# Kernel optimization log

Hardware: AMD Instinct MI355X
Metric: run time of the kernel (lower is better)

## Reference

```python
import jax, jax.numpy as jnp
import numpy as np

AXES = 72        # NUM_OF_IMU_AXES
PARAMS = 12      # NUM_OF_NOISE_PARAMS
MAX_PROP = 600   # max_propogation
LN_EPS = 1e-5    # nn.LayerNorm default eps


def setup_inputs() -> dict:
    key = jax.random.key(0)
    k0, k1 = jax.random.split(key, 2)
    S, D = 4096, 512
    hidden_states = jax.random.normal(k0, (1, S, D), jnp.float32)
    gamma = jnp.ones((D,), jnp.float32)          # LayerNorm weight
    beta = jnp.zeros((D,), jnp.float32)          # LayerNorm bias
    W = jax.random.normal(k1, (D, AXES * PARAMS), jnp.float32) * 0.02  # Linear weight (in,out)
    b = jnp.zeros((AXES * PARAMS,), jnp.float32)
    return {"hidden_states": hidden_states, "gamma": gamma, "beta": beta, "W": W, "b": b}


def reference(hidden_states, gamma, beta, W, b):
    S = hidden_states.shape[1]
    T = min(MAX_PROP, S)  # time_steps_propogate_kinematics (static under jit)

    # LayerNorm over last dim
    x = hidden_states[0]  # (S, D); B == 1 by contract
    mu = jnp.mean(x, axis=-1, keepdims=True)
    var = jnp.mean((x - mu) ** 2, axis=-1, keepdims=True)
    xn = (x - mu) / jnp.sqrt(var + LN_EPS) * gamma + beta

    # Linear -> (seq, params, axes); rearrange 'seq (params axes)' => params outer
    p = (xn @ W + b).reshape(S, PARAMS, AXES)
    sp = jax.nn.softplus

    c, c_th = p[:, 4], p[:, 5]          # (S, A)
    phi, phi_th = p[:, 6], p[:, 7]
    d = sp(p[:, 1]); k = d * d / 4 + sp(p[:, 0])
    d_th = sp(p[:, 3]); k_th = d_th * d_th / 4 + sp(p[:, 2])

    acc_base = p[:, 8].T                # (A, S)
    acc_std = sp(p[:, 9]).T
    gyro_base = p[:, 10].T
    gyro_std = sp(p[:, 11]).T

    t = jnp.arange(T, dtype=jnp.float32)[None, :, None]  # (1, T, 1)

    def osc(cc, dd, kk, ph):
        # damped oscillator value grid, vectorized over all 72 axes: (S, T, A)
        om = jnp.sqrt(4.0 * kk - dd * dd) / 2.0  # = sqrt(softplus)>=0, safe
        return (cc[:, None, :] * jnp.exp(-dd[:, None, :] / 2.0 * t)
                * jnp.sin(t * om[:, None, :] + ph[:, None, :]))

    vals = osc(c, d, k, phi) + osc(c_th, d_th, k_th, phi_th)  # (S, T, A)

    # banded overlap-add: out[s + t] += vals[s, t]; positions >= S are dropped
    pos = (jnp.arange(S)[:, None] + jnp.arange(T)[None, :]).reshape(-1)  # (S*T,)
    vals_flat = vals.reshape(S * T, AXES)
    out = jnp.zeros((S + T, AXES), vals.dtype).at[pos].add(vals_flat)[:S]  # (S, A)
    kinematics = out.T  # (A, S)

    return kinematics, acc_base, acc_std, gyro_base, gyro_std
```

## Files before the change

### kernel.cpp

```cpp
#include <hip/hip_runtime.h>
#include <math.h>

#define S_TOTAL 4096
#define DDIM    512
#define AXES    72
#define NPROJ   864
#define T_PROP  600
#define SA      (S_TOTAL*AXES)
#define LN_EPS  1e-5f
#define AMP_CUT 4e-6f

typedef __attribute__((ext_vector_type(8))) short short8;
typedef __attribute__((ext_vector_type(4))) float f32x4;

__device__ __forceinline__ float softplus_f(float x) {
    return fmaxf(x, 0.f) + log1pf(expf(-fabsf(x)));
}
__device__ __forceinline__ unsigned short bf_hi(float f) {
    return (unsigned short)(__float_as_uint(f) >> 16);
}

__global__ __launch_bounds__(256) void prep_kernel(
        const float* __restrict__ x, const float* __restrict__ gamma,
        const float* __restrict__ beta, const float* __restrict__ W,
        unsigned short* __restrict__ Ahi, unsigned short* __restrict__ Alo,
        unsigned short* __restrict__ WhiT,
        float* __restrict__ kin) {
    __shared__ float Wt[32][33];
    int tid = threadIdx.x;
    int b = blockIdx.x;
    if (b < 1024) {
        int lane = tid & 63, w = tid >> 6;
        int row = b*4 + w;
        const float4* xr = reinterpret_cast<const float4*>(x + (size_t)row * DDIM);
        float4 xv[2] = { xr[lane], xr[lane + 64] };
        float sum = 0.f, ssq = 0.f;
#pragma unroll
        for (int c = 0; c < 2; ++c) {
            sum += (xv[c].x + xv[c].y) + (xv[c].z + xv[c].w);
            ssq += xv[c].x*xv[c].x + xv[c].y*xv[c].y + xv[c].z*xv[c].z + xv[c].w*xv[c].w;
        }
#pragma unroll
        for (int off = 1; off < 64; off <<= 1) {
            sum += __shfl_xor(sum, off);
            ssq += __shfl_xor(ssq, off);
        }
        float m = sum * (1.f/DDIM);
        float r = rsqrtf(ssq * (1.f/DDIM) - m*m + LN_EPS);
        const float4* gp = reinterpret_cast<const float4*>(gamma);
        const float4* bp = reinterpret_cast<const float4*>(beta);
#pragma unroll
        for (int c = 0; c < 2; ++c) {
            float4 gv = gp[lane + 64*c], bv = bp[lane + 64*c];
            float xn[4] = {(xv[c].x-m)*r*gv.x+bv.x, (xv[c].y-m)*r*gv.y+bv.y,
                           (xv[c].z-m)*r*gv.z+bv.z, (xv[c].w-m)*r*gv.w+bv.w};
            ushort4 h4, l4;
            unsigned short* hp = &h4.x;
            unsigned short* lp = &l4.x;
#pragma unroll
            for (int j = 0; j < 4; ++j) {
                unsigned short hi = bf_hi(xn[j]);
                float fhi = __uint_as_float((unsigned)hi << 16);
                hp[j] = hi;
                lp[j] = bf_hi(xn[j] - fhi);
            }
            size_t o = (size_t)row*DDIM + 256*c + lane*4;
            *reinterpret_cast<ushort4*>(&Ahi[o]) = h4;
            *reinterpret_cast<ushort4*>(&Alo[o]) = l4;
        }
    } else if (b < 1456) {
        int wb = b - 1024;
        int bk = wb / 27, bn = wb - bk*27;
        int tx = tid & 31, ty0 = tid >> 5;
#pragma unroll
        for (int rr = 0; rr < 4; ++rr) {
            int ty = ty0 + rr*8;
            Wt[ty][tx] = W[(size_t)(bk*32 + ty)*NPROJ + bn*32 + tx];
        }
        __syncthreads();
#pragma unroll
        for (int rr = 0; rr < 4; ++rr) {
            int ny = ty0 + rr*8;
            int n = bn*32 + ny;
            int k = bk*32 + tx;
            float f = Wt[tx][ny];
            WhiT[(size_t)n*DDIM + k] = bf_hi(f);
        }
    } else {
        int zb = b - 1456;
        float4 z4 = make_float4(0.f, 0.f, 0.f, 0.f);
        float4* kp = reinterpret_cast<float4*>(kin);
#pragma unroll
        for (int i = 0; i < 8; ++i)
            kp[zb*2048 + i*256 + tid] = z4;
    }
}

__global__ __launch_bounds__(256) void gemm_kernel(
        const unsigned short* __restrict__ Ahi, const unsigned short* __restrict__ Alo,
        const unsigned short* __restrict__ WhiT,
        const float* __restrict__ bias,
        float* __restrict__ P, float* __restrict__ out) {
    __shared__ __align__(16) unsigned short ldsArena[2*10240];

    int tid  = threadIdx.x;
    int lane = tid & 63;
    int wv   = tid >> 6;
    int wm   = wv & 1;
    int wn   = wv >> 1;
    int sBase = blockIdx.x * 32;
    int nBase = blockIdx.y * 96;
    int l15 = lane & 15;
    int g   = lane >> 4;
    int r7  = l15 & 7;

    int rr = lane >> 3;
    int jj = ((lane & 7) ^ rr) * 8;
    const unsigned short* gp[5];
#pragma unroll
    for (int sg = 0; sg < 5; ++sg) {
        int seg = wv*5 + sg;
        const unsigned short* src;
        int row;
        if (seg < 8) {
            int p = seg >> 2, rg = seg & 3;
            row = sBase + rg*8 + rr;
            src = p ? Alo : Ahi;
        } else {
            int rg = seg - 8;
            row = nBase + rg*8 + rr;
            src = WhiT;
        }
        gp[sg] = src + (size_t)row*DDIM + jj;
    }

    int koff0 = (g*16) ^ (r7<<4);
    int koff1 = (64 + g*16) ^ (r7<<4);
    int rowXb = (wm*16 + l15) * 128;
    int rowWb[3];
#pragma unroll
    for (int nf = 0; nf < 3; ++nf) rowWb[nf] = (wn*48 + nf*16 + l15) * 128;

    f32x4 acc[3] = {};

#define STAGE(buf, kt) do {                                                   \
        unsigned short* lb = ldsArena + (buf)*10240 + wv*2560;                \
        _Pragma("unroll")                                                     \
        for (int sg = 0; sg < 5; ++sg)                                        \
            __builtin_amdgcn_global_load_lds(                                 \
                (const __attribute__((address_space(1))) void*)(gp[sg] + (kt)*64), \
                (__attribute__((address_space(3))) void*)(lb + sg*512),       \
                16, 0, 0);                                                    \
    } while (0)

#define COMPUTE(BUF) do {                                                     \
        const char* Bc = (const char*)ldsArena + (BUF)*20480;                 \
        _Pragma("unroll")                                                     \
        for (int kk = 0; kk < 2; ++kk) {                                      \
            int ko = kk ? koff1 : koff0;                                      \
            short8 xh, xl, wh[3];                                             \
            xh = *reinterpret_cast<const short8*>(Bc + rowXb + ko);           \
            xl = *reinterpret_cast<const short8*>(Bc + 4096 + rowXb + ko);    \
            _Pragma("unroll")                                                 \
            for (int nf = 0; nf < 3; ++nf)                                    \
                wh[nf] = *reinterpret_cast<const short8*>(Bc + 8192 + rowWb[nf] + ko); \
            _Pragma("unroll")                                                 \
            for (int nf = 0; nf < 3; ++nf)                                    \
                acc[nf] = __builtin_amdgcn_mfma_f32_16x16x32_bf16(wh[nf], xh, acc[nf], 0, 0, 0); \
            _Pragma("unroll")                                                 \
            for (int nf = 0; nf < 3; ++nf)                                    \
                acc[nf] = __builtin_amdgcn_mfma_f32_16x16x32_bf16(wh[nf], xl, acc[nf], 0, 0, 0); \
        }                                                                     \
    } while (0)

    STAGE(0, 0);
    STAGE(1, 1);

#pragma unroll 1
    for (int kt2 = 0; kt2 < 4; ++kt2) {
        asm volatile("s_waitcnt vmcnt(5)" ::: "memory");
        __builtin_amdgcn_sched_barrier(0);
        __builtin_amdgcn_s_barrier();
        COMPUTE(0);
        __builtin_amdgcn_s_barrier();
        if (kt2 < 3) STAGE(0, 2*kt2 + 2);
        if (kt2 < 3) { asm volatile("s_waitcnt vmcnt(5)" ::: "memory"); }
        else         { asm volatile("s_waitcnt vmcnt(0)" ::: "memory"); }
        __builtin_amdgcn_sched_barrier(0);
        __builtin_amdgcn_s_barrier();
        COMPUTE(1);
        __builtin_amdgcn_s_barrier();
        if (kt2 < 3) STAGE(1, 2*kt2 + 3);
    }
#undef STAGE
#undef COMPUTE

    int s = sBase + wm*16 + l15;
    int nRowBase = nBase + wn*48 + (g<<2);
#pragma unroll
    for (int nf = 0; nf < 3; ++nf) {
#pragma unroll
        for (int r = 0; r < 4; ++r) {
            int n = nRowBase + nf*16 + r;
            float val = acc[nf][r] + bias[n];
            int ip = (n * 3641) >> 18;
            int a  = n - ip * 72;
            float res;
            if (ip == 0 || ip == 2)      res = sqrtf(softplus_f(val));
            else if (ip == 1 || ip == 3 || ip == 9 || ip == 11) res = softplus_f(val);
            else                          res = val;
            float* dst = (ip < 8) ? (P + (size_t)ip * SA)
                                  : (out + (size_t)(ip - 7) * SA);
            dst[(size_t)a * S_TOTAL + s] = res;
        }
    }
}

template<int STEPS>
__device__ __forceinline__ void osc_chunk(
        float& v1a, float& v1b, float& v2a, float& v2b,
        float p1, float q1, float p2, float q2,
        float& acc0, float& acc1, int lane, int lane4) {
#pragma unroll
    for (int i = 0; i < STEPS/2; ++i) {
        {
            const int dt = 2*i;
            v1b = fmaf(p1, v1a, -(q1*v1b));
            v2b = fmaf(p2, v2a, -(q2*v2b));
            float v = v1b + v2b;
            if (dt == 0) {
                acc0 += v;
            } else {
                int addr = (lane4 + (((64-dt)&63)<<2)) & 255;
                float vr = __int_as_float(__builtin_amdgcn_ds_bpermute(addr, __float_as_int(v)));
                bool nw = lane >= dt;
                acc0 += nw ? vr : 0.f;
                acc1 += nw ? 0.f : vr;
            }
        }
        {
            const int dt = 2*i + 1;
            v1a = fmaf(p1, v1b, -(q1*v1a));
            v2a = fmaf(p2, v2b, -(q2*v2a));
            float v = v1a + v2a;
            int addr = (lane4 + (((64-dt)&63)<<2)) & 255;
            float vr = __int_as_float(__builtin_amdgcn_ds_bpermute(addr, __float_as_int(v)));
            bool nw = lane >= dt;
            acc0 += nw ? vr : 0.f;
            acc1 += nw ? 0.f : vr;
        }
    }
}

__global__ __launch_bounds__(256) void osc_kernel(const float* __restrict__ P,
                                                  float* __restrict__ kin) {
    int tid  = threadIdx.x;
    int lane = tid & 63;
    int wv   = tid >> 6;
    int lane4 = lane << 2;
    int sBase = blockIdx.x * 64;
    int a  = blockIdx.y * 2 + (wv >> 1);
    int t0 = (wv & 1) * 300;
    float t0f = (float)t0;
    if (sBase + t0 >= S_TOTAL) return;

    size_t base = (size_t)a * S_TOTAL + sBase + lane;
    float om1 = P[0*(size_t)SA + base], d1 = P[1*(size_t)SA + base];
    float om2 = P[2*(size_t)SA + base], d2 = P[3*(size_t)SA + base];
    float c1  = P[4*(size_t)SA + base], c2  = P[5*(size_t)SA + base];
    float ph1 = P[6*(size_t)SA + base], ph2 = P[7*(size_t)SA + base];

    float dcf1 = __expf(-0.5f*d1);
    float e1   = c1 * __expf(-0.5f*d1*t0f);
    float s0, c0, so, co;
    __sincosf(fmaf(t0f, om1, ph1), &s0, &c0);
    __sincosf(om1, &so, &co);
    float inv1 = __expf(0.5f*d1);
    float p1 = 2.f*dcf1*co, q1 = dcf1*dcf1;
    float v1a = e1*inv1*(s0*co - c0*so);
    float cs2 = fmaf(2.f*co, co, -1.f), sn2 = 2.f*so*co;
    float v1b = e1*inv1*inv1*(s0*cs2 - c0*sn2);
    float amp1 = fabsf(e1);
    float dq1 = q1*q1; dq1*=dq1; dq1*=dq1; dq1*=dq1; dq1*=dq1;
    float dcf2 = __expf(-0.5f*d2);
    float e2   = c2 * __expf(-0.5f*d2*t0f);
    __sincosf(fmaf(t0f, om2, ph2), &s0, &c0);
    __sincosf(om2, &so, &co);
    float inv2 = __expf(0.5f*d2);
    float p2 = 2.f*dcf2*co, q2 = dcf2*dcf2;
    float v2a = e2*inv2*(s0*co - c0*so);
    cs2 = fmaf(2.f*co, co, -1.f); sn2 = 2.f*so*co;
    float v2b = e2*inv2*inv2*(s0*cs2 - c0*sn2);
    float amp2 = fabsf(e2);
    float dq2 = q2*q2; dq2*=dq2; dq2*=dq2; dq2*=dq2; dq2*=dq2;

    float acc0 = 0.f, acc1 = 0.f;
    float* kinA = kin + (size_t)a * S_TOTAL;
    int jBase = sBase + t0;
    int ran = 0;

#pragma unroll 1
    for (int c = 0; c < 5; ++c) {
        if (__all(fmaxf(amp1, amp2) < AMP_CUT)) break;
        if (c < 4) osc_chunk<64>(v1a, v1b, v2a, v2b, p1, q1, p2, q2, acc0, acc1, lane, lane4);
        else       osc_chunk<44>(v1a, v1b, v2a, v2b, p1, q1, p2, q2, acc0, acc1, lane, lane4);
        int j = jBase + lane;
        if (j < S_TOTAL) unsafeAtomicAdd(&kinA[j], acc0);
        acc0 = acc1; acc1 = 0.f;
        jBase += 64;
        amp1 *= dq1; amp2 *= dq2;
        ran = 1;
        if (jBase >= S_TOTAL) { ran = 0; break; }
    }
    if (ran) {
        int j = jBase + lane;
        if (j < S_TOTAL) unsafeAtomicAdd(&kinA[j], acc0);
    }
}

extern "C" void kernel_launch(void* const* d_in, const int* in_sizes, int n_in,
                              void* d_out, int out_size, void* d_ws, size_t ws_size,
                              hipStream_t stream) {
    const float* x     = (const float*)d_in[0];
    const float* gamma = (const float*)d_in[1];
    const float* beta  = (const float*)d_in[2];
    const float* W     = (const float*)d_in[3];
    const float* b     = (const float*)d_in[4];
    float* out = (float*)d_out;

    unsigned char* wsb = (unsigned char*)d_ws;
    float* P    = (float*)wsb;
    unsigned short* Ahi  = (unsigned short*)(wsb + 9437184);
    unsigned short* Alo  = Ahi  + (size_t)S_TOTAL*DDIM;
    unsigned short* WhiT = Alo  + (size_t)S_TOTAL*DDIM;

    prep_kernel<<<dim3(1024 + 432 + 36), dim3(256), 0, stream>>>(x, gamma, beta, W,
                                                                 Ahi, Alo, WhiT, out);
    gemm_kernel<<<dim3(S_TOTAL/32, NPROJ/96), dim3(256), 0, stream>>>(Ahi, Alo, WhiT,
                                                                      b, P, out);
    osc_kernel<<<dim3(S_TOTAL/64, AXES/2), dim3(256), 0, stream>>>(P, out);
}
```

Before: 52.17 us.

## Split GEMM K dimension across two wave groups with LDS reduction

The GEMM block grows from 256 to 512 threads, and the two 4-wave halves each handle alternating 64-wide K chunks. Each half has its own double-buffered LDS region, so the serial K-loop is half as long. The second half writes its partial accumulators to LDS, and the first half adds them in before the bias, softplus and store epilogue. This aims to cut per-block latency and raise the number of waves in flight, at the cost of twice the LDS, an extra reduction with barriers, and half the threads sitting idle during the epilogue.

```diff
diff --git a/kernel.cpp b/kernel.cpp
--- a/kernel.cpp
+++ b/kernel.cpp
@@ -96,18 +96,20 @@
     }
 }
 
-__global__ __launch_bounds__(256) void gemm_kernel(
+__global__ __launch_bounds__(512) void gemm_kernel(
         const unsigned short* __restrict__ Ahi, const unsigned short* __restrict__ Alo,
         const unsigned short* __restrict__ WhiT,
         const float* __restrict__ bias,
         float* __restrict__ P, float* __restrict__ out) {
-    __shared__ __align__(16) unsigned short ldsArena[2*10240];
+    __shared__ __align__(16) unsigned short ldsArena[2*20480];
 
     int tid  = threadIdx.x;
     int lane = tid & 63;
     int wv   = tid >> 6;
+    int wvL  = wv & 3;
     int wm   = wv & 1;
-    int wn   = wv >> 1;
+    int wn   = (wv >> 1) & 1;
+    int wk   = wv >> 2;
     int sBase = blockIdx.x * 32;
     int nBase = blockIdx.y * 96;
     int l15 = lane & 15;
@@ -119,19 +121,19 @@
     const unsigned short* gp[5];
 #pragma unroll
     for (int sg = 0; sg < 5; ++sg) {
-        int seg = wv*5 + sg;
+        int segL = wvL*5 + sg;
         const unsigned short* src;
         int row;
-        if (seg < 8) {
-            int p = seg >> 2, rg = seg & 3;
+        if (segL < 8) {
+            int p = segL >> 2, rg = segL & 3;
             row = sBase + rg*8 + rr;
             src = p ? Alo : Ahi;
         } else {
-            int rg = seg - 8;
+            int rg = segL - 8;
             row = nBase + rg*8 + rr;
             src = WhiT;
         }
-        gp[sg] = src + (size_t)row*DDIM + jj;
+        gp[sg] = src + (size_t)row*DDIM + wk*64 + jj;
     }
 
     int koff0 = (g*16) ^ (r7<<4);
@@ -143,18 +145,18 @@
 
     f32x4 acc[3] = {};
 
-#define STAGE(buf, kt) do {                                                   \
-        unsigned short* lb = ldsArena + (buf)*10240 + wv*2560;                \
+#define STAGE(buf, c) do {                                                    \
+        unsigned short* lb = ldsArena + (buf)*20480 + wk*10240 + wvL*2560;    \
         _Pragma("unroll")                                                     \
         for (int sg = 0; sg < 5; ++sg)                                        \
             __builtin_amdgcn_global_load_lds(                                 \
-                (const __attribute__((address_space(1))) void*)(gp[sg] + (kt)*64), \
+                (const __attribute__((address_space(1))) void*)(gp[sg] + (c)*128), \
                 (__attribute__((address_space(3))) void*)(lb + sg*512),       \
                 16, 0, 0);                                                    \
     } while (0)
 
 #define COMPUTE(BUF) do {                                                     \
-        const char* Bc = (const char*)ldsArena + (BUF)*20480;                 \
+        const char* Bc = (const char*)ldsArena + (BUF)*40960 + wk*20480;      \
         _Pragma("unroll")                                                     \
         for (int kk = 0; kk < 2; ++kk) {                                      \
             int ko = kk ? koff1 : koff0;                                      \
@@ -177,41 +179,58 @@
     STAGE(1, 1);
 
 #pragma unroll 1
-    for (int kt2 = 0; kt2 < 4; ++kt2) {
+    for (int kt2 = 0; kt2 < 2; ++kt2) {
         asm volatile("s_waitcnt vmcnt(5)" ::: "memory");
         __builtin_amdgcn_sched_barrier(0);
         __builtin_amdgcn_s_barrier();
         COMPUTE(0);
         __builtin_amdgcn_s_barrier();
-        if (kt2 < 3) STAGE(0, 2*kt2 + 2);
-        if (kt2 < 3) { asm volatile("s_waitcnt vmcnt(5)" ::: "memory"); }
+        if (kt2 < 1) STAGE(0, 2);
+        if (kt2 < 1) { asm volatile("s_waitcnt vmcnt(5)" ::: "memory"); }
         else         { asm volatile("s_waitcnt vmcnt(0)" ::: "memory"); }
         __builtin_amdgcn_sched_barrier(0);
         __builtin_amdgcn_s_barrier();
         COMPUTE(1);
         __builtin_amdgcn_s_barrier();
-        if (kt2 < 3) STAGE(1, 2*kt2 + 3);
+        if (kt2 < 1) STAGE(1, 3);
     }
 #undef STAGE
 #undef COMPUTE
 
-    int s = sBase + wm*16 + l15;
-    int nRowBase = nBase + wn*48 + (g<<2);
-#pragma unroll
-    for (int nf = 0; nf < 3; ++nf) {
-#pragma unroll
-        for (int r = 0; r < 4; ++r) {
-            int n = nRowBase + nf*16 + r;
-            float val = acc[nf][r] + bias[n];
-            int ip = (n * 3641) >> 18;
-            int a  = n - ip * 72;
-            float res;
-            if (ip == 0 || ip == 2)      res = sqrtf(softplus_f(val));
-            else if (ip == 1 || ip == 3 || ip == 9 || ip == 11) res = softplus_f(val);
-            else                          res = val;
-            float* dst = (ip < 8) ? (P + (size_t)ip * SA)
-                                  : (out + (size_t)(ip - 7) * SA);
-            dst[(size_t)a * S_TOTAL + s] = res;
+    __syncthreads();
+    float* red = reinterpret_cast<float*>(ldsArena);
+    if (wk == 1) {
+        int t = tid - 256;
+#pragma unroll
+        for (int nf = 0; nf < 3; ++nf)
+            *reinterpret_cast<f32x4*>(red + t*12 + nf*4) = acc[nf];
+    }
+    __syncthreads();
+    if (wk == 0) {
+#pragma unroll
+        for (int nf = 0; nf < 3; ++nf) {
+            f32x4 o = *reinterpret_cast<const f32x4*>(red + tid*12 + nf*4);
+            acc[nf] += o;
+        }
+
+        int s = sBase + wm*16 + l15;
+        int nRowBase = nBase + wn*48 + (g<<2);
+#pragma unroll
+        for (int nf = 0; nf < 3; ++nf) {
+#pragma unroll
+            for (int r = 0; r < 4; ++r) {
+                int n = nRowBase + nf*16 + r;
+                float val = acc[nf][r] + bias[n];
+                int ip = (n * 3641) >> 18;
+                int a  = n - ip * 72;
+                float res;
+                if (ip == 0 || ip == 2)      res = sqrtf(softplus_f(val));
+                else if (ip == 1 || ip == 3 || ip == 9 || ip == 11) res = softplus_f(val);
+                else                          res = val;
+                float* dst = (ip < 8) ? (P + (size_t)ip * SA)
+                                      : (out + (size_t)(ip - 7) * SA);
+                dst[(size_t)a * S_TOTAL + s] = res;
+            }
         }
     }
 }
@@ -336,7 +355,7 @@
 
     prep_kernel<<<dim3(1024 + 432 + 36), dim3(256), 0, stream>>>(x, gamma, beta, W,
                                                                  Ahi, Alo, WhiT, out);
-    gemm_kernel<<<dim3(S_TOTAL/32, NPROJ/96), dim3(256), 0, stream>>>(Ahi, Alo, WhiT,
+    gemm_kernel<<<dim3(S_TOTAL/32, NPROJ/96), dim3(512), 0, stream>>>(Ahi, Alo, WhiT,
                                                                       b, P, out);
     osc_kernel<<<dim3(S_TOTAL/64, AXES/2), dim3(256), 0, stream>>>(P, out);
 }
```

Result: slower. 54.43 us (+4.3%).

## Replace double-buffered GEMM LDS pipeline with single-buffer load-sync-compute loop

Applied to the files above, without the earlier changes.

The GEMM kernel's double-buffered LDS staging with manual vmcnt waits and prefetch is replaced by a single LDS buffer: each k-step issues global-to-LDS loads, syncs, computes, and syncs again. This halves LDS usage per block, which may allow more resident blocks. In exchange, global loads no longer overlap MFMA compute within a block. Also, __syncthreads may not wait on outstanding global_load_lds transfers the way explicit vmcnt waits did.

```diff
diff --git a/kernel.cpp b/kernel.cpp
--- a/kernel.cpp
+++ b/kernel.cpp
@@ -101,7 +101,7 @@
         const unsigned short* __restrict__ WhiT,
         const float* __restrict__ bias,
         float* __restrict__ P, float* __restrict__ out) {
-    __shared__ __align__(16) unsigned short ldsArena[2*10240];
+    __shared__ __align__(16) unsigned short ldsArena[10240];
 
     int tid  = threadIdx.x;
     int lane = tid & 63;
@@ -143,57 +143,39 @@
 
     f32x4 acc[3] = {};
 
-#define STAGE(buf, kt) do {                                                   \
-        unsigned short* lb = ldsArena + (buf)*10240 + wv*2560;                \
-        _Pragma("unroll")                                                     \
-        for (int sg = 0; sg < 5; ++sg)                                        \
-            __builtin_amdgcn_global_load_lds(                                 \
-                (const __attribute__((address_space(1))) void*)(gp[sg] + (kt)*64), \
-                (__attribute__((address_space(3))) void*)(lb + sg*512),       \
-                16, 0, 0);                                                    \
-    } while (0)
-
-#define COMPUTE(BUF) do {                                                     \
-        const char* Bc = (const char*)ldsArena + (BUF)*20480;                 \
-        _Pragma("unroll")                                                     \
-        for (int kk = 0; kk < 2; ++kk) {                                      \
-            int ko = kk ? koff1 : koff0;                                      \
-            short8 xh, xl, wh[3];                                             \
-            xh = *reinterpret_cast<const short8*>(Bc + rowXb + ko);           \
-            xl = *reinterpret_cast<const short8*>(Bc + 4096 + rowXb + ko);    \
-            _Pragma("unroll")                                                 \
-            for (int nf = 0; nf < 3; ++nf)                                    \
-                wh[nf] = *reinterpret_cast<const short8*>(Bc + 8192 + rowWb[nf] + ko); \
-            _Pragma("unroll")                                                 \
-            for (int nf = 0; nf < 3; ++nf)                                    \
-                acc[nf] = __builtin_amdgcn_mfma_f32_16x16x32_bf16(wh[nf], xh, acc[nf], 0, 0, 0); \
-            _Pragma("unroll")                                                 \
-            for (int nf = 0; nf < 3; ++nf)                                    \
-                acc[nf] = __builtin_amdgcn_mfma_f32_16x16x32_bf16(wh[nf], xl, acc[nf], 0, 0, 0); \
-        }                                                                     \
-    } while (0)
-
-    STAGE(0, 0);
-    STAGE(1, 1);
-
 #pragma unroll 1
-    for (int kt2 = 0; kt2 < 4; ++kt2) {
-        asm volatile("s_waitcnt vmcnt(5)" ::: "memory");
-        __builtin_amdgcn_sched_barrier(0);
-        __builtin_amdgcn_s_barrier();
-        COMPUTE(0);
-        __builtin_amdgcn_s_barrier();
-        if (kt2 < 3) STAGE(0, 2*kt2 + 2);
-        if (kt2 < 3) { asm volatile("s_waitcnt vmcnt(5)" ::: "memory"); }
-        else         { asm volatile("s_waitcnt vmcnt(0)" ::: "memory"); }
-        __builtin_amdgcn_sched_barrier(0);
-        __builtin_amdgcn_s_barrier();
-        COMPUTE(1);
-        __builtin_amdgcn_s_barrier();
-        if (kt2 < 3) STAGE(1, 2*kt2 + 3);
-    }
-#undef STAGE
-#undef COMPUTE
+    for (int kt = 0; kt < 8; ++kt) {
+        {
+            unsigned short* lb = ldsArena + wv*2560;
+#pragma unroll
+            for (int sg = 0; sg < 5; ++sg)
+                __builtin_amdgcn_global_load_lds(
+                    (const __attribute__((address_space(1))) void*)(gp[sg] + kt*64),
+                    (__attribute__((address_space(3))) void*)(lb + sg*512),
+                    16, 0, 0);
+        }
+        __syncthreads();
+        {
+            const char* Bc = (const char*)ldsArena;
+#pragma unroll
+            for (int kk = 0; kk < 2; ++kk) {
+                int ko = kk ? koff1 : koff0;
+                short8 xh, xl, wh[3];
+                xh = *reinterpret_cast<const short8*>(Bc + rowXb + ko);
+                xl = *reinterpret_cast<const short8*>(Bc + 4096 + rowXb + ko);
+#pragma unroll
+                for (int nf = 0; nf < 3; ++nf)
+                    wh[nf] = *reinterpret_cast<const short8*>(Bc + 8192 + rowWb[nf] + ko);
+#pragma unroll
+                for (int nf = 0; nf < 3; ++nf)
+                    acc[nf] = __builtin_amdgcn_mfma_f32_16x16x32_bf16(wh[nf], xh, acc[nf], 0, 0, 0);
+#pragma unroll
+                for (int nf = 0; nf < 3; ++nf)
+                    acc[nf] = __builtin_amdgcn_mfma_f32_16x16x32_bf16(wh[nf], xl, acc[nf], 0, 0, 0);
+            }
+        }
+        __syncthreads();
+    }
 
     int s = sBase + wm*16 + l15;
     int nRowBase = nBase + wn*48 + (g<<2);
```

Result: slower. 53.82 us (+3.2%).

## Replace direct global-to-LDS loads with register-staged prefetch in GEMM

Applied to the files above, without the earlier changes.

The GEMM main loop no longer uses global_load_lds into double-buffered LDS with manual vmcnt waits. Each K-tile is now prefetched into registers while the current tile is computed, then written to the other LDS buffer before a single barrier per iteration. A minimum-occupancy launch bound of 4 is also added. This trades extra VGPRs and explicit LDS stores for simpler synchronization and one barrier per tile instead of several, at the risk of less load/compute overlap and register pressure under the occupancy cap.

```diff
diff --git a/kernel.cpp b/kernel.cpp
--- a/kernel.cpp
+++ b/kernel.cpp
@@ -96,7 +96,7 @@
     }
 }
 
-__global__ __launch_bounds__(256) void gemm_kernel(
+__global__ __launch_bounds__(256, 4) void gemm_kernel(
         const unsigned short* __restrict__ Ahi, const unsigned short* __restrict__ Alo,
         const unsigned short* __restrict__ WhiT,
         const float* __restrict__ bias,
@@ -142,15 +142,19 @@
     for (int nf = 0; nf < 3; ++nf) rowWb[nf] = (wn*48 + nf*16 + l15) * 128;
 
     f32x4 acc[3] = {};
-
-#define STAGE(buf, kt) do {                                                   \
-        unsigned short* lb = ldsArena + (buf)*10240 + wv*2560;                \
+    uint4 pf[5];
+
+#define LOAD(kt) do {                                                         \
         _Pragma("unroll")                                                     \
         for (int sg = 0; sg < 5; ++sg)                                        \
-            __builtin_amdgcn_global_load_lds(                                 \
-                (const __attribute__((address_space(1))) void*)(gp[sg] + (kt)*64), \
-                (__attribute__((address_space(3))) void*)(lb + sg*512),       \
-                16, 0, 0);                                                    \
+            pf[sg] = *reinterpret_cast<const uint4*>(gp[sg] + (kt)*64);       \
+    } while (0)
+
+#define COMMIT(buf) do {                                                      \
+        unsigned short* lb = ldsArena + (buf)*10240 + wv*2560 + lane*8;       \
+        _Pragma("unroll")                                                     \
+        for (int sg = 0; sg < 5; ++sg)                                        \
+            *reinterpret_cast<uint4*>(lb + sg*512) = pf[sg];                  \
     } while (0)
 
 #define COMPUTE(BUF) do {                                                     \
@@ -173,26 +177,23 @@
         }                                                                     \
     } while (0)
 
-    STAGE(0, 0);
-    STAGE(1, 1);
+    LOAD(0);
+    asm volatile("s_waitcnt vmcnt(0)" ::: "memory");
+    COMMIT(0);
+    __syncthreads();
 
 #pragma unroll 1
-    for (int kt2 = 0; kt2 < 4; ++kt2) {
-        asm volatile("s_waitcnt vmcnt(5)" ::: "memory");
-        __builtin_amdgcn_sched_barrier(0);
-        __builtin_amdgcn_s_barrier();
-        COMPUTE(0);
-        __builtin_amdgcn_s_barrier();
-        if (kt2 < 3) STAGE(0, 2*kt2 + 2);
-        if (kt2 < 3) { asm volatile("s_waitcnt vmcnt(5)" ::: "memory"); }
-        else         { asm volatile("s_waitcnt vmcnt(0)" ::: "memory"); }
-        __builtin_amdgcn_sched_barrier(0);
-        __builtin_amdgcn_s_barrier();
-        COMPUTE(1);
-        __builtin_amdgcn_s_barrier();
-        if (kt2 < 3) STAGE(1, 2*kt2 + 3);
-    }
-#undef STAGE
+    for (int kt = 0; kt < 8; ++kt) {
+        if (kt < 7) LOAD(kt + 1);
+        COMPUTE(kt & 1);
+        if (kt < 7) {
+            asm volatile("s_waitcnt vmcnt(0)" ::: "memory");
+            COMMIT((kt + 1) & 1);
+        }
+        __syncthreads();
+    }
+#undef LOAD
+#undef COMMIT
 #undef COMPUTE
 
     int s = sBase + wm*16 + l15;
```

Result: slower. 89.02 us (+70.6%).
